# Kernel tuning notes

Measured on AMD Instinct MI355X. Metric: run time of the kernel, lower is better.

The kernel has to match this reference:

```python
import jax, jax.numpy as jnp
import numpy as np

NUM_CLASSES = 80
TOPK = 1000
CONF_THRESH = 0.001
NMS_THRESH = 0.5
CLASS_OFFSET = 4096.0  # > max image coordinate, separates classes for class-aware NMS
M = 300000


def setup_inputs() -> dict:
    key = jax.random.key(0)
    k1, k2, k3, k4 = jax.random.split(key, 4)
    obj_preds = jax.random.normal(k1, (1, M, 1), dtype=jnp.float32)
    cls_preds = jax.random.normal(k2, (1, M, NUM_CLASSES), dtype=jnp.float32)
    # random xyxy boxes inside a 640x640 image
    cxcy = jax.random.uniform(k3, (1, M, 2), dtype=jnp.float32) * 640.0
    wh = jax.random.uniform(k4, (1, M, 2), dtype=jnp.float32) * 128.0 + 1.0
    box_preds = jnp.concatenate([cxcy - wh * 0.5, cxcy + wh * 0.5], axis=-1)
    return {"obj_preds": obj_preds, "cls_preds": cls_preds, "box_preds": box_preds}


def _iou_matrix(boxes):
    # boxes: [K, 4] xyxy -> [K, K] pairwise IoU
    x1, y1, x2, y2 = boxes[:, 0], boxes[:, 1], boxes[:, 2], boxes[:, 3]
    area = jnp.clip(x2 - x1, 0.0) * jnp.clip(y2 - y1, 0.0)
    xx1 = jnp.maximum(x1[:, None], x1[None, :])
    yy1 = jnp.maximum(y1[:, None], y1[None, :])
    xx2 = jnp.minimum(x2[:, None], x2[None, :])
    yy2 = jnp.minimum(y2[:, None], y2[None, :])
    inter = jnp.clip(xx2 - xx1, 0.0) * jnp.clip(yy2 - yy1, 0.0)
    return inter / (area[:, None] + area[None, :] - inter + 1e-9)


def _postprocess(obj_preds, cls_preds, box_preds):
    obj = obj_preds[0]   # [M, 1]
    cls = cls_preds[0]   # [M, C]
    box = box_preds[0]   # [M, 4]

    # sigmoid * sigmoid sqrt-score fusion (no_multi_labels branch)
    fused = jnp.sqrt(jax.nn.sigmoid(obj) * jax.nn.sigmoid(cls))  # [M, C]
    scores = jnp.max(fused, axis=1)     # [M]
    labels = jnp.argmax(fused, axis=1)  # [M]

    # sort-descending + take top-k == lax.top_k
    topk_scores, topk_idxs = jax.lax.top_k(scores, TOPK)
    labels_k = labels[topk_idxs]        # [K]
    boxes_k = box[topk_idxs]            # [K, 4]
    conf_mask = topk_scores > CONF_THRESH

    # multiclass NMS via class-offset trick (boxes of different classes never overlap)
    off = labels_k.astype(boxes_k.dtype)[:, None] * CLASS_OFFSET
    iou = _iou_matrix(boxes_k + off)    # [K, K]

    idx = jnp.arange(TOPK)

    def body(i, keep):
        # suppressed if any earlier, still-kept box overlaps > nms_thresh
        sup = (iou[i] > NMS_THRESH) & keep & (idx < i)
        return keep.at[i].set(keep[i] & ~jnp.any(sup))

    keep = jax.lax.fori_loop(0, TOPK, body, conf_mask)  # [K] bool

    keepf = keep.astype(topk_scores.dtype)
    # fixed-shape output: masked [K, 5] = (score, x1, y1, x2, y2); dropped rows zeroed
    out5 = jnp.concatenate([(topk_scores * keepf)[:, None], boxes_k * keepf[:, None]], axis=1)
    return out5, labels_k, keep


def reference(obj_preds, cls_preds, box_preds):
    return _postprocess(obj_preds, cls_preds, box_preds)
```

## Files before the change

kernel.cpp:

```cpp
#include <hip/hip_runtime.h>
#include <hip/hip_bf16.h>
#include <math.h>

#define NCLS 80
#define TOPK_N 1000
#define CAND_CAP 12288
#define T0 0.91f
#define NB 8192
#define HREP 8
#define RBINS 3072
#define RBIN_LO 0x3F680000u
#define ANCH_INV 524287

#define WS_SCORES   0
#define WS_LABELS   1200000
#define WS_CAND     2400000
#define WS_TKSCORE  2498304
#define WS_TKLABEL  2502304
#define WS_BOXES    2506304
#define WS_OBX      2522304
#define WS_AREAS    2538304
#define WS_MASK     2542304
#define WS_META     2670304
#define WS_HIST     2670368

typedef unsigned long long u64;

__device__ __forceinline__ float sigmoidf_(float x) {
    return 1.0f / (1.0f + expf(-x));
}

__device__ __forceinline__ u64 make_key(unsigned score32, int anchor, int lab) {
    return ((u64)score32 << 26) | ((u64)(ANCH_INV - anchor) << 7) | (unsigned)lab;
}

__device__ __forceinline__ int key_bin(u64 k) {
    unsigned s32 = (unsigned)(k >> 26);
    int d = (int)(s32 - RBIN_LO);
    if (d < 0) d = 0;
    int b = d >> 9;
    if (b > RBINS - 1) b = RBINS - 1;
    return (RBINS - 1) - b;
}

__device__ __forceinline__ void rowmax16(const float4* row, int l,
                                         float& bv, int& bc) {
    float4 v4 = row[l];
    bv = v4.x; bc = l * 4;
    if (v4.y > bv) { bv = v4.y; bc = l * 4 + 1; }
    if (v4.z > bv) { bv = v4.z; bc = l * 4 + 2; }
    if (v4.w > bv) { bv = v4.w; bc = l * 4 + 3; }
    if (l < 4) {
        float4 w4 = row[16 + l];
        int cb = 64 + l * 4;
        if (w4.x > bv) { bv = w4.x; bc = cb; }
        if (w4.y > bv) { bv = w4.y; bc = cb + 1; }
        if (w4.z > bv) { bv = w4.z; bc = cb + 2; }
        if (w4.w > bv) { bv = w4.w; bc = cb + 3; }
    }
    #pragma unroll
    for (int m = 8; m >= 1; m >>= 1) {
        float ov = __shfl_xor(bv, m);
        int oc = __shfl_xor(bc, m);
        if (ov > bv || (ov == bv && oc < bc)) { bv = ov; bc = oc; }
    }
}

__global__ void k1_scores(const float* __restrict__ obj,
                          const float* __restrict__ cls,
                          u64* __restrict__ cand,
                          int* __restrict__ counter, int M) {
    int wave = (blockIdx.x * 256 + threadIdx.x) >> 6;
    int lane = threadIdx.x & 63;
    int g = lane >> 4, l = lane & 15;
    int anchor = wave * 4 + g;
    if (anchor >= M) return;
    const float4* row = (const float4*)(cls + (size_t)anchor * NCLS);
    float bv; int bc;
    rowmax16(row, l, bv, bc);
    float score = 0.0f;
    if (l == 0) score = sqrtf(sigmoidf_(obj[anchor]) * sigmoidf_(bv));
    bool want = (l == 0) && (score > T0);
    u64 m = __ballot(want);
    if (want) {
        int leader = __ffsll((long long)m) - 1;
        int base = 0;
        if (lane == leader) base = atomicAdd(counter, (int)__popcll(m));
        base = __shfl(base, leader);
        int pos = base + (int)__popcll(m & ((1ULL << lane) - 1ULL));
        if (pos < CAND_CAP)
            cand[pos] = make_key(__float_as_uint(score), anchor, bc);
    }
}

__global__ void kf_hist(const float* __restrict__ obj,
                        const float* __restrict__ cls,
                        float* __restrict__ scores,
                        int* __restrict__ labels,
                        unsigned* __restrict__ hist,
                        const int* __restrict__ meta, int M) {
    int C = meta[2];
    if (C >= TOPK_N && C <= CAND_CAP) return;
    int gw = (blockIdx.x * 256 + threadIdx.x) >> 6;
    int TW = gridDim.x * 4;
    int lane = threadIdx.x & 63;
    int g = lane >> 4, l = lane & 15;
    int rep = blockIdx.x & (HREP - 1);
    for (int a0 = gw * 4; a0 < M; a0 += TW * 4) {
        int anchor = a0 + g;
        if (anchor >= M) continue;
        const float4* row = (const float4*)(cls + (size_t)anchor * NCLS);
        float bv; int bc;
        rowmax16(row, l, bv, bc);
        if (l == 0) {
            float score = sqrtf(sigmoidf_(obj[anchor]) * sigmoidf_(bv));
            scores[anchor] = score;
            labels[anchor] = bc;
            atomicAdd(&hist[(size_t)rep * NB + (__float_as_uint(score) >> 17)], 1u);
        }
    }
}

__global__ void k2_scan(const unsigned* __restrict__ hist, int* __restrict__ meta) {
    int C = meta[2];
    if (C >= TOPK_N && C <= CAND_CAP) return;
    int t = threadIdx.x;
    int lane = t & 63, w = t >> 6;
    int base = NB - 1 - t * 8;
    unsigned bins[8]; unsigned s = 0;
    #pragma unroll
    for (int k = 0; k < 8; ++k) {
        unsigned h = 0;
        for (int r = 0; r < HREP; ++r) h += hist[(size_t)r * NB + base - k];
        bins[k] = h; s += h;
    }
    unsigned inc = s;
    for (int d = 1; d < 64; d <<= 1) {
        unsigned pv = __shfl_up(inc, d);
        if (lane >= d) inc += pv;
    }
    __shared__ unsigned wsum[16], woff[16];
    if (lane == 63) wsum[w] = inc;
    __syncthreads();
    if (t == 0) {
        unsigned cum = 0;
        for (int i = 0; i < 16; ++i) { woff[i] = cum; cum += wsum[i]; }
    }
    __syncthreads();
    unsigned excl = woff[w] + inc - s;
    if (excl < TOPK_N && excl + s >= TOPK_N) {
        unsigned cum = excl; int b = base;
        #pragma unroll
        for (int k = 0; k < 8; ++k) {
            unsigned h = bins[k];
            if (cum + h >= TOPK_N) { meta[0] = b; break; }
            cum += h; --b;
        }
    }
}

__global__ void k3_compact(const float* __restrict__ scores,
                           const int* __restrict__ labels,
                           int* __restrict__ meta,
                           u64* __restrict__ cand, int M) {
    int C = meta[2];
    if (C >= TOPK_N && C <= CAND_CAP) return;
    int B = meta[0];
    for (int i = blockIdx.x * 256 + threadIdx.x; i < M; i += gridDim.x * 256) {
        unsigned key = __float_as_uint(scores[i]);
        if ((int)(key >> 17) >= B) {
            int pos = atomicAdd(meta + 3, 1);
            if (pos < CAND_CAP)
                cand[pos] = make_key(key, i, labels[i]);
        }
    }
}

__global__ void __launch_bounds__(1024)
k4_rank(const u64* __restrict__ cand,
        const int* __restrict__ meta,
        const float4* __restrict__ box,
        float* __restrict__ tkscore,
        int* __restrict__ tklabel,
        float4* __restrict__ boxes_k,
        float4* __restrict__ obx,
        float* __restrict__ areas) {
    __shared__ u64 sorted[CAND_CAP];
    __shared__ unsigned hist[RBINS];
    __shared__ unsigned cnt[RBINS];
    __shared__ unsigned wsum[16], woff[16];
    int t = threadIdx.x;
    int lane = t & 63, w = t >> 6;
    int Cf = meta[2];
    bool fast = (Cf >= TOPK_N && Cf <= CAND_CAP);
    int C = fast ? Cf : meta[3];
    if (C > CAND_CAP) C = CAND_CAP;
    for (int b = t; b < RBINS; b += 1024) { hist[b] = 0; cnt[b] = 0; }
    __syncthreads();
    u64 keys[12]; int nk = 0;
    for (int i = t; i < C; i += 1024) {
        u64 k = cand[i];
        keys[nk++] = k;
        atomicAdd(&hist[key_bin(k)], 1u);
    }
    __syncthreads();
    unsigned h0 = hist[t * 3], h1 = hist[t * 3 + 1], h2 = hist[t * 3 + 2];
    unsigned s = h0 + h1 + h2;
    unsigned inc = s;
    for (int d = 1; d < 64; d <<= 1) {
        unsigned pv = __shfl_up(inc, d);
        if (lane >= d) inc += pv;
    }
    if (lane == 63) wsum[w] = inc;
    __syncthreads();
    if (t == 0) {
        unsigned cum = 0;
        for (int i = 0; i < 16; ++i) { woff[i] = cum; cum += wsum[i]; }
    }
    __syncthreads();
    unsigned base = woff[w] + inc - s;
    hist[t * 3] = base;
    hist[t * 3 + 1] = base + h0;
    hist[t * 3 + 2] = base + h0 + h1;
    __syncthreads();
    nk = 0;
    for (int i = t; i < C; i += 1024) {
        u64 k = keys[nk++];
        int b = key_bin(k);
        unsigned pos = hist[b] + atomicAdd(&cnt[b], 1u);
        sorted[pos] = k;
    }
    __syncthreads();
    for (int p = t; p < C; p += 1024) {
        u64 k = sorted[p];
        int b = key_bin(k);
        unsigned b0 = hist[b], b1 = b0 + cnt[b];
        int r = (int)b0;
        for (unsigned q = b0; q < b1; ++q) r += (sorted[q] > k);
        if (r < TOPK_N) {
            unsigned s32 = (unsigned)(k >> 26);
            int anchor = ANCH_INV - (int)((k >> 7) & 0x7FFFF);
            int lab = (int)(k & 127u);
            float sc = __uint_as_float(s32);
            tkscore[r] = sc;
            tklabel[r] = lab;
            float4 bb = box[anchor];
            boxes_k[r] = bb;
            float off = (float)lab * 4096.0f;
            float4 ob = make_float4(bb.x + off, bb.y + off, bb.z + off, bb.w + off);
            obx[r] = ob;
            areas[r] = fmaxf(ob.z - ob.x, 0.0f) * fmaxf(ob.w - ob.y, 0.0f);
        }
    }
}

__global__ void k5_iou(const float4* __restrict__ obx,
                       const float* __restrict__ areas,
                       u64* __restrict__ mask) {
    int i = blockIdx.x * 4 + (threadIdx.x >> 6);
    int lane = threadIdx.x & 63;
    if (i >= TOPK_N) return;
    float4 bi = obx[i];
    float ai = areas[i];
    for (int w = 0; w < 16; ++w) {
        int c = w * 64 + lane;
        bool bit = false;
        if (c < i) {
            float4 bc = obx[c];
            float xx1 = fmaxf(bi.x, bc.x), yy1 = fmaxf(bi.y, bc.y);
            float xx2 = fminf(bi.z, bc.z), yy2 = fminf(bi.w, bc.w);
            float inter = fmaxf(xx2 - xx1, 0.0f) * fmaxf(yy2 - yy1, 0.0f);
            float iou = inter / (ai + areas[c] - inter + 1e-9f);
            bit = iou > 0.5f;
        }
        u64 bal = __ballot(bit);
        if (lane == 0) mask[(size_t)i * 16 + w] = bal;
    }
}

__global__ void __launch_bounds__(1024)
k6_nms(const float* __restrict__ tkscore,
       const u64* __restrict__ mask,
       const int* __restrict__ tklabel,
       const float4* __restrict__ boxes_k,
       float* __restrict__ out) {
    __shared__ u64 kept_s[16], dec_s[16];
    int t = threadIdx.x, w = t >> 6, lane = t & 63;
    bool active = t < TOPK_N;
    u64 sup[16];
    float sc = 0.0f;
    if (active) {
        #pragma unroll
        for (int q = 0; q < 16; ++q) sup[q] = mask[(size_t)t * 16 + q];
        sc = tkscore[t];
    } else {
        #pragma unroll
        for (int q = 0; q < 16; ++q) sup[q] = 0ULL;
    }
    bool conf = active && (sc > 0.001f);
    bool mydec = !conf;
    bool mykept = false;
    u64 db = __ballot(mydec), kb = __ballot(mykept);
    if (lane == 0) { dec_s[w] = db; kept_s[w] = kb; }
    __syncthreads();
    for (int round = 0; round < TOPK_N; ++round) {
        if (!mydec) {
            u64 pend = 0;
            #pragma unroll
            for (int q = 0; q < 16; ++q) pend |= sup[q] & ~dec_s[q];
            if (pend == 0ULL) {
                u64 kk = 0;
                #pragma unroll
                for (int q = 0; q < 16; ++q) kk |= sup[q] & kept_s[q];
                mydec = true; mykept = (kk == 0ULL);
            }
        }
        __syncthreads();
        db = __ballot(mydec); kb = __ballot(mykept);
        if (lane == 0) { dec_s[w] = db; kept_s[w] = kb; }
        __syncthreads();
        u64 a = ~0ULL;
        #pragma unroll
        for (int q = 0; q < 16; ++q) a &= dec_s[q];
        if (a == ~0ULL) break;
    }
    if (active) {
        float k = mykept ? 1.0f : 0.0f;
        float4 b = boxes_k[t];
        out[t * 5 + 0] = sc * k;
        out[t * 5 + 1] = b.x * k;
        out[t * 5 + 2] = b.y * k;
        out[t * 5 + 3] = b.z * k;
        out[t * 5 + 4] = b.w * k;
        out[5 * TOPK_N + t] = (float)tklabel[t];
        out[6 * TOPK_N + t] = k;
    }
}

extern "C" void kernel_launch(void* const* d_in, const int* in_sizes, int n_in,
                              void* d_out, int out_size, void* d_ws, size_t ws_size,
                              hipStream_t stream) {
    const float* obj = (const float*)d_in[0];
    const float* cls = (const float*)d_in[1];
    const float* box = (const float*)d_in[2];
    float* out = (float*)d_out;
    char* ws = (char*)d_ws;
    int M = in_sizes[0];

    float*    scores  = (float*)(ws + WS_SCORES);
    int*      labels  = (int*)(ws + WS_LABELS);
    u64*      cand    = (u64*)(ws + WS_CAND);
    float*    tkscore = (float*)(ws + WS_TKSCORE);
    int*      tklabel = (int*)(ws + WS_TKLABEL);
    float4*   boxes_k = (float4*)(ws + WS_BOXES);
    float4*   obx     = (float4*)(ws + WS_OBX);
    float*    areas   = (float*)(ws + WS_AREAS);
    u64*      mask    = (u64*)(ws + WS_MASK);
    int*      meta    = (int*)(ws + WS_META);
    unsigned* hist    = (unsigned*)(ws + WS_HIST);

    hipMemsetAsync(ws + WS_META, 0, 64 + (size_t)HREP * NB * 4, stream);

    k1_scores<<<(M + 15) / 16, 256, 0, stream>>>(obj, cls, cand, meta + 2, M);
    kf_hist<<<512, 256, 0, stream>>>(obj, cls, scores, labels, hist, meta, M);
    k2_scan<<<1, 1024, 0, stream>>>(hist, meta);
    k3_compact<<<512, 256, 0, stream>>>(scores, labels, meta, cand, M);
    k4_rank<<<1, 1024, 0, stream>>>(cand, meta, (const float4*)box,
                                    tkscore, tklabel, boxes_k, obx, areas);
    k5_iou<<<(TOPK_N + 3) / 4, 256, 0, stream>>>(obx, areas, mask);
    k6_nms<<<1, 1024, 0, stream>>>(tkscore, mask, tklabel, boxes_k, out);
}
```

Baseline: 200.8 us.

## Defer argmax label to top-k gather and batch candidate writes per block

The first pass now computes only the row max (no argmax), with each 16-lane group handling four anchors, and gathers above-threshold keys in shared memory before a single global atomic per block. The label field is dropped from the sort key and the labels array is removed. A new small kernel recomputes the argmax for only the final 1000 top-k anchors and gathers boxes, offset boxes and areas. This cuts per-anchor work and global atomics in the dominant full scan, at the cost of one extra launch and a re-read of 1000 class rows. Argmax tie-breaking is now applied only at gather time, which gives the same result.

```diff
diff --git a/kernel.cpp b/kernel.cpp
--- a/kernel.cpp
+++ b/kernel.cpp
@@ -13,16 +13,16 @@
 #define ANCH_INV 524287
 
 #define WS_SCORES   0
-#define WS_LABELS   1200000
-#define WS_CAND     2400000
-#define WS_TKSCORE  2498304
-#define WS_TKLABEL  2502304
-#define WS_BOXES    2506304
-#define WS_OBX      2522304
-#define WS_AREAS    2538304
-#define WS_MASK     2542304
-#define WS_META     2670304
-#define WS_HIST     2670368
+#define WS_CAND     1200000
+#define WS_TKSCORE  1298304
+#define WS_TKANCH   1302304
+#define WS_TKLABEL  1306304
+#define WS_BOXES    1310304
+#define WS_OBX      1326304
+#define WS_AREAS    1342304
+#define WS_MASK     1346304
+#define WS_META     1474304
+#define WS_HIST     1474368
 
 typedef unsigned long long u64;
 
@@ -30,12 +30,12 @@
     return 1.0f / (1.0f + expf(-x));
 }
 
-__device__ __forceinline__ u64 make_key(unsigned score32, int anchor, int lab) {
-    return ((u64)score32 << 26) | ((u64)(ANCH_INV - anchor) << 7) | (unsigned)lab;
+__device__ __forceinline__ u64 make_key2(unsigned s32, int anchor) {
+    return ((u64)s32 << 19) | (unsigned)(ANCH_INV - anchor);
 }
 
 __device__ __forceinline__ int key_bin(u64 k) {
-    unsigned s32 = (unsigned)(k >> 26);
+    unsigned s32 = (unsigned)(k >> 19);
     int d = (int)(s32 - RBIN_LO);
     if (d < 0) d = 0;
     int b = d >> 9;
@@ -66,37 +66,63 @@
     }
 }
 
-__global__ void k1_scores(const float* __restrict__ obj,
-                          const float* __restrict__ cls,
-                          u64* __restrict__ cand,
-                          int* __restrict__ counter, int M) {
-    int wave = (blockIdx.x * 256 + threadIdx.x) >> 6;
-    int lane = threadIdx.x & 63;
-    int g = lane >> 4, l = lane & 15;
-    int anchor = wave * 4 + g;
-    if (anchor >= M) return;
-    const float4* row = (const float4*)(cls + (size_t)anchor * NCLS);
-    float bv; int bc;
-    rowmax16(row, l, bv, bc);
-    float score = 0.0f;
-    if (l == 0) score = sqrtf(sigmoidf_(obj[anchor]) * sigmoidf_(bv));
-    bool want = (l == 0) && (score > T0);
-    u64 m = __ballot(want);
-    if (want) {
-        int leader = __ffsll((long long)m) - 1;
-        int base = 0;
-        if (lane == leader) base = atomicAdd(counter, (int)__popcll(m));
-        base = __shfl(base, leader);
-        int pos = base + (int)__popcll(m & ((1ULL << lane) - 1ULL));
-        if (pos < CAND_CAP)
-            cand[pos] = make_key(__float_as_uint(score), anchor, bc);
+__global__ void __launch_bounds__(256)
+k1_scores(const float* __restrict__ obj,
+          const float* __restrict__ cls,
+          u64* __restrict__ cand,
+          int* __restrict__ counter, int M) {
+    __shared__ int lcount, lbase;
+    __shared__ u64 lkeys[64];
+    int t = threadIdx.x;
+    if (t == 0) lcount = 0;
+    __syncthreads();
+    int l = t & 15;
+    int grp = t >> 4;
+    int base = blockIdx.x * 64 + grp * 4;
+    if (base < M) {
+        const float4* p = (const float4*)(cls + (size_t)base * NCLS);
+        float4 a0 = p[l], a1 = p[20 + l], a2 = p[40 + l], a3 = p[60 + l];
+        float m0 = fmaxf(fmaxf(a0.x, a0.y), fmaxf(a0.z, a0.w));
+        float m1 = fmaxf(fmaxf(a1.x, a1.y), fmaxf(a1.z, a1.w));
+        float m2 = fmaxf(fmaxf(a2.x, a2.y), fmaxf(a2.z, a2.w));
+        float m3 = fmaxf(fmaxf(a3.x, a3.y), fmaxf(a3.z, a3.w));
+        if (l < 4) {
+            float4 b0 = p[16 + l], b1 = p[36 + l], b2 = p[56 + l], b3 = p[76 + l];
+            m0 = fmaxf(m0, fmaxf(fmaxf(b0.x, b0.y), fmaxf(b0.z, b0.w)));
+            m1 = fmaxf(m1, fmaxf(fmaxf(b1.x, b1.y), fmaxf(b1.z, b1.w)));
+            m2 = fmaxf(m2, fmaxf(fmaxf(b2.x, b2.y), fmaxf(b2.z, b2.w)));
+            m3 = fmaxf(m3, fmaxf(fmaxf(b3.x, b3.y), fmaxf(b3.z, b3.w)));
+        }
+        #pragma unroll
+        for (int s = 8; s >= 1; s >>= 1) {
+            m0 = fmaxf(m0, __shfl_xor(m0, s));
+            m1 = fmaxf(m1, __shfl_xor(m1, s));
+            m2 = fmaxf(m2, __shfl_xor(m2, s));
+            m3 = fmaxf(m3, __shfl_xor(m3, s));
+        }
+        if (l < 4) {
+            float mm = (l < 2) ? ((l == 0) ? m0 : m1) : ((l == 2) ? m2 : m3);
+            int anchor = base + l;
+            float score = sqrtf(sigmoidf_(obj[anchor]) * sigmoidf_(mm));
+            if (score > T0) {
+                int pos = atomicAdd(&lcount, 1);
+                lkeys[pos] = make_key2(__float_as_uint(score), anchor);
+            }
+        }
+    }
+    __syncthreads();
+    if (t == 0 && lcount > 0) lbase = atomicAdd(counter, lcount);
+    __syncthreads();
+    int n = lcount;
+    if (t < n) {
+        int pos = lbase + t;
+        if (pos < CAND_CAP) cand[pos] = lkeys[t];
     }
 }
 
 __global__ void kf_hist(const float* __restrict__ obj,
                         const float* __restrict__ cls,
                         float* __restrict__ scores,
-                        int* __restrict__ labels,
                         unsigned* __restrict__ hist,
                         const int* __restrict__ meta, int M) {
     int C = meta[2];
@@ -115,7 +141,6 @@
         if (l == 0) {
             float score = sqrtf(sigmoidf_(obj[anchor]) * sigmoidf_(bv));
             scores[anchor] = score;
-            labels[anchor] = bc;
             atomicAdd(&hist[(size_t)rep * NB + (__float_as_uint(score) >> 17)], 1u);
         }
     }
@@ -160,7 +185,6 @@
 }
 
 __global__ void k3_compact(const float* __restrict__ scores,
-                           const int* __restrict__ labels,
                            int* __restrict__ meta,
                            u64* __restrict__ cand, int M) {
     int C = meta[2];
@@ -171,7 +195,7 @@
         if ((int)(key >> 17) >= B) {
             int pos = atomicAdd(meta + 3, 1);
             if (pos < CAND_CAP)
-                cand[pos] = make_key(key, i, labels[i]);
+                cand[pos] = make_key2(key, i);
         }
     }
 }
@@ -179,12 +203,8 @@
 __global__ void __launch_bounds__(1024)
 k4_rank(const u64* __restrict__ cand,
         const int* __restrict__ meta,
-        const float4* __restrict__ box,
         float* __restrict__ tkscore,
-        int* __restrict__ tklabel,
-        float4* __restrict__ boxes_k,
-        float4* __restrict__ obx,
-        float* __restrict__ areas) {
+        int* __restrict__ tkanchor) {
     __shared__ u64 sorted[CAND_CAP];
     __shared__ unsigned hist[RBINS];
     __shared__ unsigned cnt[RBINS];
@@ -238,19 +258,35 @@
         int r = (int)b0;
         for (unsigned q = b0; q < b1; ++q) r += (sorted[q] > k);
         if (r < TOPK_N) {
-            unsigned s32 = (unsigned)(k >> 26);
-            int anchor = ANCH_INV - (int)((k >> 7) & 0x7FFFF);
-            int lab = (int)(k & 127u);
-            float sc = __uint_as_float(s32);
-            tkscore[r] = sc;
-            tklabel[r] = lab;
-            float4 bb = box[anchor];
-            boxes_k[r] = bb;
-            float off = (float)lab * 4096.0f;
-            float4 ob = make_float4(bb.x + off, bb.y + off, bb.z + off, bb.w + off);
-            obx[r] = ob;
-            areas[r] = fmaxf(ob.z - ob.x, 0.0f) * fmaxf(ob.w - ob.y, 0.0f);
-        }
+            tkscore[r] = __uint_as_float((unsigned)(k >> 19));
+            tkanchor[r] = ANCH_INV - (int)(k & 0x7FFFF);
+        }
+    }
+}
+
+__global__ void __launch_bounds__(256)
+k4b_gather(const float* __restrict__ cls,
+           const float4* __restrict__ box,
+           const int* __restrict__ tkanchor,
+           int* __restrict__ tklabel,
+           float4* __restrict__ boxes_k,
+           float4* __restrict__ obx,
+           float* __restrict__ areas) {
+    int grp = threadIdx.x >> 4, l = threadIdx.x & 15;
+    int r = blockIdx.x * 16 + grp;
+    if (r >= TOPK_N) return;
+    int anchor = tkanchor[r];
+    const float4* row = (const float4*)(cls + (size_t)anchor * NCLS);
+    float bv; int bc;
+    rowmax16(row, l, bv, bc);
+    if (l == 0) {
+        tklabel[r] = bc;
+        float4 b = box[anchor];
+        boxes_k[r] = b;
+        float off = (float)bc * 4096.0f;
+        float4 ob = make_float4(b.x + off, b.y + off, b.z + off, b.w + off);
+        obx[r] = ob;
+        areas[r] = fmaxf(ob.z - ob.x, 0.0f) * fmaxf(ob.w - ob.y, 0.0f);
     }
 }
 
@@ -348,9 +384,9 @@
     int M = in_sizes[0];
 
     float*    scores  = (float*)(ws + WS_SCORES);
-    int*      labels  = (int*)(ws + WS_LABELS);
     u64*      cand    = (u64*)(ws + WS_CAND);
     float*    tkscore = (float*)(ws + WS_TKSCORE);
+    int*      tkanch  = (int*)(ws + WS_TKANCH);
     int*      tklabel = (int*)(ws + WS_TKLABEL);
     float4*   boxes_k = (float4*)(ws + WS_BOXES);
     float4*   obx     = (float4*)(ws + WS_OBX);
@@ -361,12 +397,13 @@
 
     hipMemsetAsync(ws + WS_META, 0, 64 + (size_t)HREP * NB * 4, stream);
 
-    k1_scores<<<(M + 15) / 16, 256, 0, stream>>>(obj, cls, cand, meta + 2, M);
-    kf_hist<<<512, 256, 0, stream>>>(obj, cls, scores, labels, hist, meta, M);
+    k1_scores<<<(M + 63) / 64, 256, 0, stream>>>(obj, cls, cand, meta + 2, M);
+    kf_hist<<<512, 256, 0, stream>>>(obj, cls, scores, hist, meta, M);
     k2_scan<<<1, 1024, 0, stream>>>(hist, meta);
-    k3_compact<<<512, 256, 0, stream>>>(scores, labels, meta, cand, M);
-    k4_rank<<<1, 1024, 0, stream>>>(cand, meta, (const float4*)box,
-                                    tkscore, tklabel, boxes_k, obx, areas);
+    k3_compact<<<512, 256, 0, stream>>>(scores, meta, cand, M);
+    k4_rank<<<1, 1024, 0, stream>>>(cand, meta, tkscore, tkanch);
+    k4b_gather<<<(TOPK_N + 15) / 16, 256, 0, stream>>>(cls, (const float4*)box,
+                                                       tkanch, tklabel, boxes_k, obx, areas);
     k5_iou<<<(TOPK_N + 3) / 4, 256, 0, stream>>>(obx, areas, mask);
     k6_nms<<<1, 1024, 0, stream>>>(tkscore, mask, tklabel, boxes_k, out);
 }
```

Result: faster. 190.4 us (-5.2%).
